# Kernel optimization log

Hardware: AMD Instinct MI355X
Metric: run time of the kernel (lower is better)

## Reference

```python
import jax, jax.numpy as jnp
import numpy as np

IN, H, C, B = 1024, 1024, 16, 4096


def setup_inputs() -> dict:
    key = jax.random.key(0)
    ks = jax.random.split(key, 5)
    s = 1.0 / np.sqrt(IN)
    sh = 1.0 / np.sqrt(H)
    return {
        "input_word": jax.random.normal(ks[0], (B, IN), dtype=jnp.float32),
        "hidden_states": jax.random.normal(ks[1], (B, H), dtype=jnp.float32),
        # stacked per-cell Linear weights (torch Linear: y = x @ W.T + b)
        "Wx": jax.random.uniform(ks[2], (C, 2 * H, IN), jnp.float32, -s, s),
        "bx": jax.random.uniform(ks[3], (C, 2 * H), jnp.float32, -s, s),
        "Wh": jax.random.uniform(ks[4], (C, 2 * H, H), jnp.float32, -sh, sh),
    }


def reference(input_word, hidden_states, Wx, bx, Wh):
    # all cells active (entity_mask all ones, domain_tag='Source')
    # net[b,c,o] = sum_i x[b,i] Wx[c,o,i] + bx[c,o] + sum_h h[b,h] Wh[c,o,h]
    net = (jnp.einsum('bi,coi->bco', input_word, Wx)
           + jnp.einsum('bh,coh->bco', hidden_states, Wh)
           + bx[None, :, :])  # [B, C, 2H]
    input_gate, cell_states = net[..., :H], net[..., H:]
    cell_input = jnp.tanh(cell_states)
    input_gate = jax.nn.sigmoid(input_gate)
    return (cell_input, input_gate)
```

## Files before the change

### kernel.cpp

```cpp
#include <hip/hip_runtime.h>
#include <hip/hip_bf16.h>

#define IN_DIM 1024
#define H_DIM  1024
#define C_DIM  16
#define B_DIM  4096
#define K_DIM  2048
#define N_DIM  32768
#define M_DIM  4096
#define NT     32

typedef __attribute__((ext_vector_type(8))) short short8;
typedef __attribute__((ext_vector_type(4))) float f32x4;

__device__ __forceinline__ unsigned short f2bf_rne(float f) {
  union { float f; unsigned u; } a; a.f = f;
  unsigned r = a.u + 0x7FFFu + ((a.u >> 16) & 1u);
  return (unsigned short)(r >> 16);
}

__global__ void convert_pack_kernel(const float* __restrict__ xs,
                                    const float* __restrict__ hs,
                                    unsigned short* __restrict__ out,
                                    int rows) {
  long total = (long)rows * (K_DIM / 8);
  for (long i = blockIdx.x * (long)blockDim.x + threadIdx.x; i < total;
       i += (long)gridDim.x * blockDim.x) {
    long e = i * 8;
    int r = (int)(e >> 11);
    int k = (int)(e & 2047);
    const float* src = (k < IN_DIM) ? (xs + (long)r * IN_DIM + k)
                                    : (hs + (long)r * H_DIM + (k - IN_DIM));
    float4 v0 = *(const float4*)(src);
    float4 v1 = *(const float4*)(src + 4);
    union { unsigned short u[8]; short8 s; } p;
    p.u[0] = f2bf_rne(v0.x); p.u[1] = f2bf_rne(v0.y);
    p.u[2] = f2bf_rne(v0.z); p.u[3] = f2bf_rne(v0.w);
    p.u[4] = f2bf_rne(v1.x); p.u[5] = f2bf_rne(v1.y);
    p.u[6] = f2bf_rne(v1.z); p.u[7] = f2bf_rne(v1.w);
    *(short8*)(out + e) = p.s;
  }
}

__device__ __forceinline__ void dma16(const short* g, int ldsOff) {
  asm volatile("s_mov_b32 m0, %1\n\t"
               "global_load_lds_dwordx4 %0, off"
               :: "v"(g), "s"(ldsOff) : "memory");
}

__global__ void __launch_bounds__(512, 2)
gemm_act_kernel(const short* __restrict__ A,
                const short* __restrict__ Bt,
                const float* __restrict__ bias,
                float* __restrict__ out) {
  extern __shared__ short lds[];

  int cpx = (int)gridDim.x >> 3;
  int wg  = ((int)blockIdx.x & 7) * cpx + ((int)blockIdx.x >> 3);
  int mt = wg & 15;
  int nt = wg >> 4;
  int m0 = mt * 256;
  int n0 = nt * 256;

  const int tid  = (int)threadIdx.x;
  const int lane = tid & 63;
  const int wid  = tid >> 6;
  const int wr   = wid >> 2;
  const int wc   = wid & 3;

  const int crow = (lane >> 4) * 4;
  const int ccol = lane & 15;
  const long HALF = (long)B_DIM * C_DIM * H_DIM;
  float bia[4]; int cg[4], og[4];
#pragma unroll
  for (int ni = 0; ni < 4; ++ni) {
    int gn = n0 + wc * 64 + ni * 16 + ccol;
    bia[ni] = bias[gn];
    cg[ni] = gn >> 11;
    og[ni] = gn & 2047;
  }

  const int srow = tid >> 3;
  const int sc   = (tid & 7) ^ (srow & 7);
  const short* Abase = A  + (long)(m0 + srow) * K_DIM + sc * 8;
  const short* Bbase = Bt + (long)(n0 + srow) * K_DIM + sc * 8;
  const int wb = __builtin_amdgcn_readfirstlane((tid >> 6) * 1024);

  auto stA = [&](int kt, int r0, int buf) {
    dma16(Abase + (long)r0 * K_DIM + kt * 64, buf * 32768 + r0 * 128 + wb);
  };
  auto stB = [&](int kt, int r0, int buf) {
    dma16(Bbase + (long)r0 * K_DIM + kt * 64, 65536 + buf * 32768 + r0 * 128 + wb);
  };

  const int fr = lane & 15;
  const int g8 = lane >> 4;
  int aoff0[2], boff0[2];
#pragma unroll
  for (int kk = 0; kk < 2; ++kk) {
    aoff0[kk] = (wr * 128 + fr) * 64 + (((kk * 4 + g8) ^ (fr & 7)) << 3);
    boff0[kk] = (wc * 64  + fr) * 64 + (((kk * 4 + g8) ^ (fr & 7)) << 3);
  }
  auto lda = [&](int buf, int mi, int kk) {
    return *(const short8*)(lds + buf * 16384 + aoff0[kk] + mi * 1024);
  };
  auto ldb = [&](int buf, int ni, int kk) {
    return *(const short8*)(lds + 32768 + buf * 16384 + boff0[kk] + ni * 1024);
  };

  f32x4 acc[8][4] = {};
  short8 avA[4], avB[4], bv0[4], bv1[4];

  auto mfma4 = [&](short8 (&a)[4], short8 (&b)[4], int mb) {
#pragma unroll
    for (int i = 0; i < 4; ++i)
#pragma unroll
      for (int j = 0; j < 4; ++j)
        acc[mb + i][j] = __builtin_amdgcn_mfma_f32_16x16x32_bf16(a[i], b[j], acc[mb + i][j], 0, 0, 0);
  };

  stA(0, 0, 0); stA(0, 64, 0); stA(0, 128, 0); stA(0, 192, 0);
  stB(0, 0, 0); stB(0, 64, 0); stB(0, 128, 0); stB(0, 192, 0);
  stB(1, 0, 1); stB(1, 64, 1); stB(1, 128, 1); stB(1, 192, 1);
  stA(1, 0, 1); stA(1, 128, 1);
  asm volatile("s_waitcnt vmcnt(6)" ::: "memory");
  __builtin_amdgcn_s_barrier();
#pragma unroll
  for (int i = 0; i < 4; ++i) avA[i] = lda(0, i, 0);
#pragma unroll
  for (int j = 0; j < 4; ++j) bv0[j] = ldb(0, j, 0);

  auto iter = [&](int t, int cur, int nx) {
    const int t1 = (t + 1 < NT) ? t + 1 : NT - 1;
    const int t2 = (t + 2 < NT) ? t + 2 : NT - 1;
#pragma unroll
    for (int i = 0; i < 4; ++i) avB[i] = lda(cur, i, 1);
#pragma unroll
    for (int j = 0; j < 4; ++j) bv1[j] = ldb(cur, j, 1);
    stA(t1, 64, nx);
    __builtin_amdgcn_s_setprio(1);
    mfma4(avA, bv0, 0);
    __builtin_amdgcn_s_setprio(0);
    asm volatile("s_waitcnt vmcnt(7)" ::: "memory");
    __builtin_amdgcn_s_barrier();
#pragma unroll
    for (int i = 0; i < 4; ++i) avA[i] = lda(cur, 4 + i, 0);
    stA(t1, 192, nx);
    __builtin_amdgcn_s_setprio(1);
    mfma4(avB, bv1, 0);
    __builtin_amdgcn_s_setprio(0);
    __builtin_amdgcn_s_barrier();
#pragma unroll
    for (int i = 0; i < 4; ++i) avB[i] = lda(cur, 4 + i, 1);
    stB(t2, 0, cur); stB(t2, 64, cur); stA(t2, 0, cur);
    __builtin_amdgcn_s_setprio(1);
    mfma4(avA, bv0, 4);
    __builtin_amdgcn_s_setprio(0);
    asm volatile("s_waitcnt vmcnt(5)" ::: "memory");
    __builtin_amdgcn_s_barrier();
#pragma unroll
    for (int i = 0; i < 4; ++i) avA[i] = lda(nx, i, 0);
#pragma unroll
    for (int j = 0; j < 4; ++j) bv0[j] = ldb(nx, j, 0);
    stB(t2, 128, cur); stB(t2, 192, cur); stA(t2, 128, cur);
    __builtin_amdgcn_s_setprio(1);
    mfma4(avB, bv1, 4);
    __builtin_amdgcn_s_setprio(0);
    __builtin_amdgcn_s_barrier();
  };

  for (int t = 0; t < NT; t += 2) {
    iter(t,     0, 1);
    iter(t + 1, 1, 0);
  }
  asm volatile("s_waitcnt vmcnt(0)" ::: "memory");

#pragma unroll
  for (int mi = 0; mi < 8; ++mi) {
    int gb0 = m0 + wr * 128 + mi * 16 + crow;
#pragma unroll
    for (int ni = 0; ni < 4; ++ni) {
      int c = cg[ni], o = og[ni];
#pragma unroll
      for (int j = 0; j < 4; ++j) {
        float v = acc[mi][ni][j] + bia[ni];
        long b = gb0 + j;
        if (o < H_DIM) {
          float r = 1.0f / (1.0f + __expf(-v));
          __builtin_nontemporal_store(r, &out[HALF + (b * C_DIM + c) * H_DIM + o]);
        } else {
          float av2 = fabsf(v);
          float e = __expf(-2.0f * av2);
          float r = (1.0f - e) / (1.0f + e);
          r = (v < 0.0f) ? -r : r;
          __builtin_nontemporal_store(r, &out[(b * C_DIM + c) * H_DIM + (o - H_DIM)]);
        }
      }
    }
  }
}

__global__ void fallback_kernel(const float* __restrict__ x,
                                const float* __restrict__ h,
                                const float* __restrict__ Wx,
                                const float* __restrict__ bx,
                                const float* __restrict__ Wh,
                                float* __restrict__ out) {
  int b = blockIdx.x;
  int c = blockIdx.y;
  __shared__ float lx[IN_DIM], lh[H_DIM];
  for (int i = threadIdx.x; i < IN_DIM; i += blockDim.x) {
    lx[i] = x[(long)b * IN_DIM + i];
    lh[i] = h[(long)b * H_DIM + i];
  }
  __syncthreads();
  const long HALF = (long)B_DIM * C_DIM * H_DIM;
  for (int o = threadIdx.x; o < 2 * H_DIM; o += blockDim.x) {
    const float* wx = Wx + ((long)c * 2 * H_DIM + o) * IN_DIM;
    const float* wh = Wh + ((long)c * 2 * H_DIM + o) * H_DIM;
    float acc = bx[c * 2 * H_DIM + o];
    for (int k = 0; k < IN_DIM; ++k) acc += lx[k] * wx[k];
    for (int k = 0; k < H_DIM; ++k) acc += lh[k] * wh[k];
    if (o < H_DIM) {
      out[HALF + ((long)b * C_DIM + c) * H_DIM + o] = 1.0f / (1.0f + __expf(-acc));
    } else {
      float av = fabsf(acc);
      float t = __expf(-2.0f * av);
      float r = (1.0f - t) / (1.0f + t);
      out[((long)b * C_DIM + c) * H_DIM + (o - H_DIM)] = (acc < 0.0f) ? -r : r;
    }
  }
}

extern "C" void kernel_launch(void* const* d_in, const int* in_sizes, int n_in,
                              void* d_out, int out_size, void* d_ws, size_t ws_size,
                              hipStream_t stream) {
  const float* x  = (const float*)d_in[0];
  const float* h  = (const float*)d_in[1];
  const float* Wx = (const float*)d_in[2];
  const float* bx = (const float*)d_in[3];
  const float* Wh = (const float*)d_in[4];
  float* out = (float*)d_out;

  const size_t needA = (size_t)M_DIM * K_DIM * sizeof(short);
  const size_t needB = (size_t)N_DIM * K_DIM * sizeof(short);
  if (ws_size < needA + needB) {
    dim3 g(B_DIM, C_DIM);
    fallback_kernel<<<g, 256, 0, stream>>>(x, h, Wx, bx, Wh, out);
    return;
  }

  unsigned short* Abf = (unsigned short*)d_ws;
  unsigned short* Bbf = (unsigned short*)((char*)d_ws + needA);

  convert_pack_kernel<<<2048, 256, 0, stream>>>(x, h, Abf, M_DIM);
  convert_pack_kernel<<<4096, 256, 0, stream>>>(Wx, Wh, Bbf, N_DIM);

  (void)hipFuncSetAttribute((const void*)gemm_act_kernel,
                            hipFuncAttributeMaxDynamicSharedMemorySize, 131072);
  gemm_act_kernel<<<2048, 512, 131072, stream>>>((const short*)Abf, (const short*)Bbf,
                                                 bx, out);
}
```

Before: 709.9 us.

## Restructure GEMM main loop into ping-pong schedule with barrier-separated LDS reads and MFMA

Replaces the four-phase iteration lambda with an explicitly unrolled eight-phase loop over two LDS buffers. Each phase alternates a block of LDS fragment reads plus staggered global-to-LDS DMA issues with a barrier-fenced MFMA block, and uses fixed byte offsets instead of buffer indices. The aim is to spread DMA issue and memory waits more evenly and to keep warps in lockstep, ping-pong style, so memory and MFMA work interleave across waves. The cost is roughly twice as many barriers per K-tile, and the changed vmcnt accounting risks stalls or a race if the counts are wrong.

```diff
diff --git a/kernel.cpp b/kernel.cpp
--- a/kernel.cpp
+++ b/kernel.cpp
@@ -86,31 +86,29 @@
   const short* Bbase = Bt + (long)(n0 + srow) * K_DIM + sc * 8;
   const int wb = __builtin_amdgcn_readfirstlane((tid >> 6) * 1024);
 
-  auto stA = [&](int kt, int r0, int buf) {
-    dma16(Abase + (long)r0 * K_DIM + kt * 64, buf * 32768 + r0 * 128 + wb);
-  };
-  auto stB = [&](int kt, int r0, int buf) {
-    dma16(Bbase + (long)r0 * K_DIM + kt * 64, 65536 + buf * 32768 + r0 * 128 + wb);
+  auto stA = [&](int kt, int r0, int bufByte) {
+    dma16(Abase + (long)r0 * K_DIM + kt * 64, bufByte + r0 * 128 + wb);
+  };
+  auto stB = [&](int kt, int r0, int bufByte) {
+    dma16(Bbase + (long)r0 * K_DIM + kt * 64, 65536 + bufByte + r0 * 128 + wb);
   };
 
   const int fr = lane & 15;
   const int g8 = lane >> 4;
-  int aoff0[2], boff0[2];
+  int aoff[2], boff[2];
 #pragma unroll
   for (int kk = 0; kk < 2; ++kk) {
-    aoff0[kk] = (wr * 128 + fr) * 64 + (((kk * 4 + g8) ^ (fr & 7)) << 3);
-    boff0[kk] = (wc * 64  + fr) * 64 + (((kk * 4 + g8) ^ (fr & 7)) << 3);
-  }
-  auto lda = [&](int buf, int mi, int kk) {
-    return *(const short8*)(lds + buf * 16384 + aoff0[kk] + mi * 1024);
-  };
-  auto ldb = [&](int buf, int ni, int kk) {
-    return *(const short8*)(lds + 32768 + buf * 16384 + boff0[kk] + ni * 1024);
+    aoff[kk] = (wr * 128 + fr) * 64 + (((kk * 4 + g8) ^ (fr & 7)) << 3);
+    boff[kk] = (wc * 64  + fr) * 64 + (((kk * 4 + g8) ^ (fr & 7)) << 3);
+  }
+  auto rdA = [&](int baseS, int mi, int kk) {
+    return *(const short8*)(lds + baseS + aoff[kk] + mi * 1024);
+  };
+  auto rdB = [&](int baseS, int ni, int kk) {
+    return *(const short8*)(lds + baseS + boff[kk] + ni * 1024);
   };
 
   f32x4 acc[8][4] = {};
-  short8 avA[4], avB[4], bv0[4], bv1[4];
-
   auto mfma4 = [&](short8 (&a)[4], short8 (&b)[4], int mb) {
 #pragma unroll
     for (int i = 0; i < 4; ++i)
@@ -119,59 +117,92 @@
         acc[mb + i][j] = __builtin_amdgcn_mfma_f32_16x16x32_bf16(a[i], b[j], acc[mb + i][j], 0, 0, 0);
   };
 
-  stA(0, 0, 0); stA(0, 64, 0); stA(0, 128, 0); stA(0, 192, 0);
-  stB(0, 0, 0); stB(0, 64, 0); stB(0, 128, 0); stB(0, 192, 0);
-  stB(1, 0, 1); stB(1, 64, 1); stB(1, 128, 1); stB(1, 192, 1);
-  stA(1, 0, 1); stA(1, 128, 1);
-  asm volatile("s_waitcnt vmcnt(6)" ::: "memory");
+  stA(0, 0, 0);      stA(0, 64, 0);      stA(0, 128, 0);      stA(0, 192, 0);
+  stB(0, 0, 0);      stB(0, 64, 0);      stB(0, 128, 0);      stB(0, 192, 0);
+  stA(1, 0, 32768);  stA(1, 128, 32768);
+  stB(1, 0, 32768);  stB(1, 64, 32768);
+  asm volatile("s_waitcnt vmcnt(4)" ::: "memory");
   __builtin_amdgcn_s_barrier();
-#pragma unroll
-  for (int i = 0; i < 4; ++i) avA[i] = lda(0, i, 0);
-#pragma unroll
-  for (int j = 0; j < 4; ++j) bv0[j] = ldb(0, j, 0);
-
-  auto iter = [&](int t, int cur, int nx) {
-    const int t1 = (t + 1 < NT) ? t + 1 : NT - 1;
+
+  for (int t = 0; t < NT; t += 2) {
+    const int t1 = t + 1;
     const int t2 = (t + 2 < NT) ? t + 2 : NT - 1;
-#pragma unroll
-    for (int i = 0; i < 4; ++i) avB[i] = lda(cur, i, 1);
-#pragma unroll
-    for (int j = 0; j < 4; ++j) bv1[j] = ldb(cur, j, 1);
-    stA(t1, 64, nx);
-    __builtin_amdgcn_s_setprio(1);
-    mfma4(avA, bv0, 0);
-    __builtin_amdgcn_s_setprio(0);
-    asm volatile("s_waitcnt vmcnt(7)" ::: "memory");
-    __builtin_amdgcn_s_barrier();
-#pragma unroll
-    for (int i = 0; i < 4; ++i) avA[i] = lda(cur, 4 + i, 0);
-    stA(t1, 192, nx);
-    __builtin_amdgcn_s_setprio(1);
-    mfma4(avB, bv1, 0);
-    __builtin_amdgcn_s_setprio(0);
-    __builtin_amdgcn_s_barrier();
-#pragma unroll
-    for (int i = 0; i < 4; ++i) avB[i] = lda(cur, 4 + i, 1);
-    stB(t2, 0, cur); stB(t2, 64, cur); stA(t2, 0, cur);
-    __builtin_amdgcn_s_setprio(1);
-    mfma4(avA, bv0, 4);
-    __builtin_amdgcn_s_setprio(0);
-    asm volatile("s_waitcnt vmcnt(5)" ::: "memory");
-    __builtin_amdgcn_s_barrier();
-#pragma unroll
-    for (int i = 0; i < 4; ++i) avA[i] = lda(nx, i, 0);
-#pragma unroll
-    for (int j = 0; j < 4; ++j) bv0[j] = ldb(nx, j, 0);
-    stB(t2, 128, cur); stB(t2, 192, cur); stA(t2, 128, cur);
-    __builtin_amdgcn_s_setprio(1);
-    mfma4(avB, bv1, 4);
-    __builtin_amdgcn_s_setprio(0);
-    __builtin_amdgcn_s_barrier();
-  };
-
-  for (int t = 0; t < NT; t += 2) {
-    iter(t,     0, 1);
-    iter(t + 1, 1, 0);
+    const int t3 = (t + 3 < NT) ? t + 3 : NT - 1;
+    short8 av[4], bv0[4], bv1[4];
+#pragma unroll
+    for (int i = 0; i < 4; ++i) av[i] = rdA(0, i, 0);
+#pragma unroll
+    for (int j = 0; j < 4; ++j) bv0[j] = rdB(32768, j, 0);
+    stA(t1, 64, 32768); stA(t1, 192, 32768);
+    stB(t1, 128, 32768); stB(t1, 192, 32768);
+    __builtin_amdgcn_s_barrier();
+    __builtin_amdgcn_s_setprio(1);
+    mfma4(av, bv0, 0);
+    __builtin_amdgcn_s_setprio(0);
+    __builtin_amdgcn_s_barrier();
+#pragma unroll
+    for (int i = 0; i < 4; ++i) av[i] = rdA(0, i, 1);
+#pragma unroll
+    for (int j = 0; j < 4; ++j) bv1[j] = rdB(32768, j, 1);
+    __builtin_amdgcn_s_barrier();
+    __builtin_amdgcn_s_setprio(1);
+    mfma4(av, bv1, 0);
+    __builtin_amdgcn_s_setprio(0);
+    __builtin_amdgcn_s_barrier();
+#pragma unroll
+    for (int i = 0; i < 4; ++i) av[i] = rdA(0, 4 + i, 0);
+    stA(t2, 0, 0); stA(t2, 128, 0);
+    __builtin_amdgcn_s_barrier();
+    __builtin_amdgcn_s_setprio(1);
+    mfma4(av, bv0, 4);
+    __builtin_amdgcn_s_setprio(0);
+    __builtin_amdgcn_s_barrier();
+#pragma unroll
+    for (int i = 0; i < 4; ++i) av[i] = rdA(0, 4 + i, 1);
+    stB(t2, 0, 0); stB(t2, 64, 0);
+    asm volatile("s_waitcnt vmcnt(4)" ::: "memory");
+    __builtin_amdgcn_s_barrier();
+    __builtin_amdgcn_s_setprio(1);
+    mfma4(av, bv1, 4);
+    __builtin_amdgcn_s_setprio(0);
+    __builtin_amdgcn_s_barrier();
+#pragma unroll
+    for (int i = 0; i < 4; ++i) av[i] = rdA(16384, i, 0);
+#pragma unroll
+    for (int j = 0; j < 4; ++j) bv0[j] = rdB(49152, j, 0);
+    stA(t2, 64, 0); stA(t2, 192, 0);
+    stB(t2, 128, 0); stB(t2, 192, 0);
+    __builtin_amdgcn_s_barrier();
+    __builtin_amdgcn_s_setprio(1);
+    mfma4(av, bv0, 0);
+    __builtin_amdgcn_s_setprio(0);
+    __builtin_amdgcn_s_barrier();
+#pragma unroll
+    for (int i = 0; i < 4; ++i) av[i] = rdA(16384, i, 1);
+#pragma unroll
+    for (int j = 0; j < 4; ++j) bv1[j] = rdB(49152, j, 1);
+    __builtin_amdgcn_s_barrier();
+    __builtin_amdgcn_s_setprio(1);
+    mfma4(av, bv1, 0);
+    __builtin_amdgcn_s_setprio(0);
+    __builtin_amdgcn_s_barrier();
+#pragma unroll
+    for (int i = 0; i < 4; ++i) av[i] = rdA(16384, 4 + i, 0);
+    stA(t3, 0, 32768); stA(t3, 128, 32768);
+    __builtin_amdgcn_s_barrier();
+    __builtin_amdgcn_s_setprio(1);
+    mfma4(av, bv0, 4);
+    __builtin_amdgcn_s_setprio(0);
+    __builtin_amdgcn_s_barrier();
+#pragma unroll
+    for (int i = 0; i < 4; ++i) av[i] = rdA(16384, 4 + i, 1);
+    stB(t3, 0, 32768); stB(t3, 64, 32768);
+    asm volatile("s_waitcnt vmcnt(4)" ::: "memory");
+    __builtin_amdgcn_s_barrier();
+    __builtin_amdgcn_s_setprio(1);
+    mfma4(av, bv1, 4);
+    __builtin_amdgcn_s_setprio(0);
+    __builtin_amdgcn_s_barrier();
   }
   asm volatile("s_waitcnt vmcnt(0)" ::: "memory");
 
```

After: 769.3 us. +8.4%, slower.
